# Optimization experiments

Hardware: AMD Instinct MI355X
Metric: run time of the kernel (lower is better)

## Reference

```python
import jax, jax.numpy as jnp
import numpy as np

B, N, H, DK, DV = 2, 2048, 16, 128, 128
E = H * DV
EPS = 1e-6


def setup_inputs() -> dict:
    key = jax.random.key(0)
    ks = jax.random.split(key, 8)
    sc_qk = 1.0 / np.sqrt(E + H * DK)  # xavier_normal-ish std
    sc_e = 1.0 / np.sqrt(2 * E)
    d = {
        "x": jax.random.normal(ks[0], (B, N, E), jnp.float32),
        "Wq": jax.random.normal(ks[1], (H * DK, E), jnp.float32) * sc_qk,
        "bq": jnp.zeros((H * DK,), jnp.float32),
        "Wk": jax.random.normal(ks[2], (H * DK, E), jnp.float32) * sc_qk,
        "bk": jnp.zeros((H * DK,), jnp.float32),
        "Wv": jax.random.normal(ks[3], (E, E), jnp.float32) * sc_e,
        "bv": jnp.zeros((E,), jnp.float32),
        "Wg": jax.random.normal(ks[4], (E, E), jnp.float32) * sc_e,
        "bg": jnp.zeros((E,), jnp.float32),
        "Wo": jax.random.normal(ks[5], (E, E), jnp.float32) * sc_e,
        "bo": jnp.zeros((E,), jnp.float32),
        "start_idx": 0,
    }
    return d


def _retention_scan(q, k, v, decays):
    # q,k: [B,N,H,DK] (k already scaled), v: [B,N,H,DV]
    qs = jnp.moveaxis(q, 1, 0)  # [N,B,H,DK]
    ks_ = jnp.moveaxis(k, 1, 0)
    vs = jnp.moveaxis(v, 1, 0)
    dec = decays[None, :, None, None]  # [1,H,1,1]

    def step(state, qkv):
        qt, kt, vt = qkv
        # state_n = decay * state_{n-1} + k_n (x) v_n
        state = dec * state + kt[..., :, None] * vt[..., None, :]  # [B,H,DK,DV]
        ret = jnp.einsum("bhk,bhkv->bhv", qt, state)
        return state, ret

    init = jnp.zeros((q.shape[0], H, DK, DV), q.dtype)
    final_state, rets = jax.lax.scan(step, init, (qs, ks_, vs))
    return jnp.moveaxis(rets, 0, 1), final_state  # [B,N,H,DV], [B,H,DK,DV]


def reference(x, Wq, bq, Wk, bk, Wv, bv, Wg, bg, Wo, bo, start_idx):
    b, n, _ = x.shape
    decays = 1.0 - jnp.exp2(-5.0 - jnp.arange(H, dtype=jnp.float32))  # [H]
    q = (x @ Wq.T + bq).reshape(b, n, H, DK)
    k = (x @ Wk.T + bk).reshape(b, n, H, DK) / (DK ** 0.5)
    v = (x @ Wv.T + bv).reshape(b, n, H, DV)
    retention, state = _retention_scan(q, k, v, decays)
    # GroupNorm over (b n) tokens, num_groups=H, channels=E, no affine
    r = retention.reshape(b * n, H, DV).astype(jnp.float32)
    mu = jnp.mean(r, axis=-1, keepdims=True)
    var = jnp.var(r, axis=-1, keepdims=True)
    r = (r - mu) / jnp.sqrt(var + EPS)
    r = r.reshape(b, n, E).astype(x.dtype)
    gate = jax.nn.silu(x @ Wg.T + bg)
    out = (r * gate) @ Wo.T + bo
    return out, state
```

## Files before the change

### kernel.cpp

```cpp
#include <hip/hip_runtime.h>
#include <hip/hip_bf16.h>

typedef __attribute__((ext_vector_type(8))) short short8;
typedef __attribute__((ext_vector_type(4))) short short4v;
typedef __attribute__((ext_vector_type(4))) float floatx4;

#define DI __device__ __forceinline__

constexpr int B_ = 2, N_ = 2048, H_ = 16, DK_ = 128, DV_ = 128, E_ = 2048;
constexpr int M_ = B_ * N_;
constexpr int NCAT_ = 4 * E_;
constexpr int CH_ = 128;
constexpr int NC_ = N_ / CH_;
constexpr float KSCALE = 0.08838834764831845f;

constexpr long OFF_XB   = 0;
constexpr long OFF_WCAT = 16777216;
constexpr long OFF_WOB  = 50331648;
constexpr long OFF_BCAT = 58720256;
constexpr long OFF_Y    = 58753024;
constexpr long OFF_KT   = 125861888;
constexpr long OFF_VT   = 142639104;
constexpr long OFF_SCB  = 159416320;

DI unsigned short f2bf(float f){
  unsigned u = __float_as_uint(f);
  u += 0x7fffu + ((u >> 16) & 1u);
  return (unsigned short)(u >> 16);
}
DI float bf2f(unsigned short s){ return __uint_as_float(((unsigned)s) << 16); }

DI void gload_lds16(const void* g, void* l){
  __builtin_amdgcn_global_load_lds(
      (const __attribute__((address_space(1))) unsigned int*)g,
      (__attribute__((address_space(3))) unsigned int*)l, 16, 0, 0);
}

__global__ void k_castall(const float* __restrict__ x,
                          const float* __restrict__ Wq, const float* __restrict__ Wk,
                          const float* __restrict__ Wv, const float* __restrict__ Wg,
                          const float* __restrict__ Wo,
                          const float* __restrict__ bq, const float* __restrict__ bk,
                          const float* __restrict__ bv, const float* __restrict__ bg,
                          unsigned short* __restrict__ xb, unsigned short* __restrict__ Wcat,
                          unsigned short* __restrict__ Wob, float* __restrict__ bcat){
  int bid = blockIdx.x;
  if(bid >= 14336){
    int i = (bid - 14336) * 2048 + threadIdx.x * 8;
    #pragma unroll
    for(int u=0;u<8;++u){
      int j = i + u;
      float v;
      if(j < 2048)      v = bq[j];
      else if(j < 4096) v = bk[j - 2048];
      else if(j < 6144) v = bv[j - 4096];
      else              v = bg[j - 6144];
      bcat[j] = v;
    }
    return;
  }
  const float* s; unsigned short* d; long off;
  if(bid < 4096){ s = x; d = xb; off = (long)bid*2048; }
  else if(bid < 6144){ s = Wq; d = Wcat;            off = (long)(bid-4096)*2048; }
  else if(bid < 8192){ s = Wk; d = Wcat + 4194304L; off = (long)(bid-6144)*2048; }
  else if(bid < 10240){ s = Wv; d = Wcat + 8388608L; off = (long)(bid-8192)*2048; }
  else if(bid < 12288){ s = Wg; d = Wcat + 12582912L; off = (long)(bid-10240)*2048; }
  else { s = Wo; d = Wob; off = (long)(bid-12288)*2048; }
  long i = off + (long)threadIdx.x * 8;
  float4 v0 = *(const float4*)(s + i);
  float4 v1 = *(const float4*)(s + i + 4);
  short8 o;
  o[0]=(short)f2bf(v0.x); o[1]=(short)f2bf(v0.y); o[2]=(short)f2bf(v0.z); o[3]=(short)f2bf(v0.w);
  o[4]=(short)f2bf(v1.x); o[5]=(short)f2bf(v1.y); o[6]=(short)f2bf(v1.z); o[7]=(short)f2bf(v1.w);
  *(short8*)(d + i) = o;
}

__global__ __launch_bounds__(512, 2)
void k_gemm256(const unsigned short* __restrict__ A,
               const unsigned short* __restrict__ Bt,
               unsigned short* __restrict__ Y,
               const float* __restrict__ bias)
{
  extern __shared__ unsigned short lds[];
  constexpr int K = 2048;
  constexpr int NKT = K / 64;

  const int tid = threadIdx.x;
  const int wave = tid >> 6, lane = tid & 63;
  const int wr = wave >> 2, wc = wave & 3;
  const int l15 = lane & 15;

  int bid = blockIdx.x;
  int g = bid & 7, w = bid >> 3;
  int bm = (g & 1) * 8 + (w & 7);
  int bn = (g >> 1) * 8 + (w >> 3);

  const unsigned short* Ag = A  + (long)bm * 256 * K;
  const unsigned short* Bg = Bt + (long)bn * 256 * K;

  const int sr = (lane >> 3);
  const int sc = ((lane & 7) ^ sr) * 8;
  const int colx[2] = { ((0 + (lane>>4)) ^ (lane&7)) << 4,
                        ((4 + (lane>>4)) ^ (lane&7)) << 4 };

  floatx4 acc[8][4] = {};
  const char* ldsc = (const char*)lds;

  short8 Aa[8], Ab[8], Ba[4], Bb[4];

#define STG(buf, kt) do{                                                              \
    _Pragma("unroll")                                                                 \
    for(int s=0;s<4;++s){                                                             \
      const int _i = wave*4 + s;                                                      \
      gload_lds16(Ag + (long)(_i*8 + sr)*K + (long)(kt)*64 + sc,                      \
                  &lds[(buf)*16384 + _i*512 + lane*8]);                               \
      gload_lds16(Bg + (long)(_i*8 + sr)*K + (long)(kt)*64 + sc,                      \
                  &lds[32768 + (buf)*16384 + _i*512 + lane*8]);                       \
    }                                                                                 \
  }while(0)

#define RD_A(dst, cbuf, mh) do{                                                       \
    const char* _b = ldsc + (cbuf)*32768;                                             \
    _Pragma("unroll")                                                                 \
    for(int ai=0;ai<4;++ai){                                                          \
      const int _rb = (wr*128 + (mh)*64 + ai*16 + l15) << 7;                          \
      dst[ai*2+0] = *(const short8*)(_b + _rb + colx[0]);                             \
      dst[ai*2+1] = *(const short8*)(_b + _rb + colx[1]);                             \
    }                                                                                 \
  }while(0)

#define RD_B(dst, cbuf, nh) do{                                                       \
    const char* _b = ldsc + 65536 + (cbuf)*32768;                                     \
    _Pragma("unroll")                                                                 \
    for(int bj=0;bj<2;++bj){                                                          \
      const int _rb = (wc*64 + (nh)*32 + bj*16 + l15) << 7;                           \
      dst[bj*2+0] = *(const short8*)(_b + _rb + colx[0]);                             \
      dst[bj*2+1] = *(const short8*)(_b + _rb + colx[1]);                             \
    }                                                                                 \
  }while(0)

#define MFQ(mh, nh, As, Bs) do{                                                       \
    __builtin_amdgcn_s_setprio(1);                                                    \
    _Pragma("unroll")                                                                 \
    for(int ai=0;ai<4;++ai)                                                           \
      _Pragma("unroll")                                                               \
      for(int bj=0;bj<2;++bj)                                                         \
        _Pragma("unroll")                                                             \
        for(int kk=0;kk<2;++kk)                                                       \
          acc[(mh)*4+ai][(nh)*2+bj] = __builtin_amdgcn_mfma_f32_16x16x32_bf16(        \
              As[ai*2+kk], Bs[bj*2+kk], acc[(mh)*4+ai][(nh)*2+bj], 0,0,0);            \
    __builtin_amdgcn_s_setprio(0);                                                    \
  }while(0)

#define SBAR  __builtin_amdgcn_s_barrier()
#define SCHED __builtin_amdgcn_sched_barrier(0)

  STG(0, 0);
  STG(1, 1);
  asm volatile("s_waitcnt vmcnt(8)" ::: "memory");
  SBAR;
  RD_A(Aa, 0, 0);
  RD_B(Ba, 0, 0);
  SCHED;

  #pragma unroll 1
  for(int u=0; u<NKT; ++u){
    const int cur = u & 1, nxt = cur ^ 1;

    RD_A(Ab, cur, 1);
    RD_B(Bb, cur, 1);
    SCHED;
    SBAR;
    MFQ(0, 0, Aa, Ba);
    SBAR; SCHED;

    MFQ(0, 1, Aa, Bb);
    SBAR; SCHED;

    MFQ(1, 0, Ab, Ba);
    asm volatile("s_waitcnt vmcnt(0)" ::: "memory");
    SBAR; SCHED;

    STG(cur, (u + 2) & (NKT - 1));
    RD_A(Aa, nxt, 0);
    RD_B(Ba, nxt, 0);
    SCHED;
    MFQ(1, 1, Ab, Bb);
    SCHED;
  }
#undef STG
#undef RD_A
#undef RD_B
#undef MFQ
#undef SBAR
#undef SCHED

  #pragma unroll
  for(int mh=0;mh<2;++mh){
    #pragma unroll
    for(int ai=0;ai<4;++ai){
      const int rowi = bm*256 + wr*128 + mh*64 + ai*16 + ((lane>>4)<<2);
      #pragma unroll
      for(int nh=0;nh<2;++nh){
        #pragma unroll
        for(int bj=0;bj<2;++bj){
          const int col = bn*256 + wc*64 + nh*32 + bj*16 + l15;
          const float bs = bias[col];
          const int sec = col >> 11;
          #pragma unroll
          for(int r=0;r<4;++r){
            float v = acc[mh*4+ai][nh*2+bj][r] + bs;
            if(sec == 1) v *= KSCALE;
            else if(sec == 3) v = v / (1.f + __expf(-v));
            Y[(long)(rowi + r) * NCAT_ + col] = f2bf(v);
          }
        }
      }
    }
  }
}

template<int EPI>
__global__ __launch_bounds__(256)
void k_gemm(const unsigned short* __restrict__ A,
            const unsigned short* __restrict__ Bt,
            void* __restrict__ outp,
            const float* __restrict__ bias,
            int M, int Ncols, int K, int NB)
{
  __shared__ unsigned short lA[2*128*64];
  __shared__ unsigned short lB[2*128*64];
  const int bid = blockIdx.x;
  const int bm = bid / NB, bn = bid % NB;
  const int tid = threadIdx.x;
  const int wave = tid >> 6, lane = tid & 63;
  const int wr = wave >> 1, wc = wave & 1;

  floatx4 acc[4][4] = {};

  int srow[4], scol[4];
  #pragma unroll
  for(int is=0; is<4; ++is){
    int o = is*4096 + wave*1024 + lane*16;
    int row = o >> 7;
    int logcb = (o & 127) ^ ((row & 7) << 4);
    srow[is] = row; scol[is] = logcb >> 1;
  }
  const unsigned short* Abase = A + (long)bm * 128 * K;
  const unsigned short* Bbase = Bt + (long)bn * 128 * K;

#define STG128(kt, buf) do{                                                          \
    const int _k0 = (kt) << 6;                                                       \
    _Pragma("unroll")                                                                \
    for(int is=0; is<4; ++is){                                                       \
      gload_lds16(Abase + (long)srow[is]*K + _k0 + scol[is], &lA[(buf)*8192 + ((is*4096 + wave*1024) >> 1)]); \
      gload_lds16(Bbase + (long)srow[is]*K + _k0 + scol[is], &lB[(buf)*8192 + ((is*4096 + wave*1024) >> 1)]); \
    }                                                                                \
  }while(0)

  const int nkt = K >> 6;
  STG128(0, 0);
  for(int kt=0; kt<nkt; ++kt){
    const int cur = kt & 1, nxt = cur ^ 1;
    const int ktn = (kt + 1 == nkt) ? 0 : kt + 1;
    __syncthreads();
    STG128(ktn, nxt);
    const char* cA = (const char*)lA + cur*16384;
    const char* cB = (const char*)lB + cur*16384;
    #pragma unroll
    for(int kk=0; kk<2; ++kk){
      const int cb = (kk<<6) + ((lane>>4)<<4);
      short8 af[4], bfr[4];
      #pragma unroll
      for(int i=0;i<4;++i){
        int row = (wr<<6) + (i<<4) + (lane&15);
        af[i] = *(const short8*)(cA + (row<<7) + (cb ^ ((row&7)<<4)));
      }
      #pragma unroll
      for(int j=0;j<4;++j){
        int row = (wc<<6) + (j<<4) + (lane&15);
        bfr[j] = *(const short8*)(cB + (row<<7) + (cb ^ ((row&7)<<4)));
      }
      #pragma unroll
      for(int i=0;i<4;++i)
        #pragma unroll
        for(int j=0;j<4;++j)
          acc[i][j] = __builtin_amdgcn_mfma_f32_16x16x32_bf16(af[i], bfr[j], acc[i][j], 0,0,0);
    }
  }
#undef STG128

  #pragma unroll
  for(int i=0;i<4;++i){
    #pragma unroll
    for(int j=0;j<4;++j){
      #pragma unroll
      for(int r=0;r<4;++r){
        int row = bm*128 + (wr<<6) + (i<<4) + ((lane>>4)<<2) + r;
        int col = bn*128 + (wc<<6) + (j<<4) + (lane&15);
        float v = acc[i][j][r] + bias[col];
        if(EPI == 0){
          int sec = col >> 11;
          if(sec == 1) v *= KSCALE;
          else if(sec == 3) v = v / (1.f + __expf(-v));
          ((unsigned short*)outp)[(long)row * Ncols + col] = f2bf(v);
        } else {
          ((float*)outp)[(long)row * Ncols + col] = v;
        }
      }
    }
  }
}

__global__ __launch_bounds__(256)
void k_transpose(const unsigned short* __restrict__ Y,
                 unsigned short* __restrict__ Kt, unsigned short* __restrict__ Vt){
  __shared__ unsigned short lt[128][136];
  int bid = blockIdx.x;
  int op = bid >> 9;
  int r  = bid & 511;
  int bh = r >> 4, c = r & 15, b = bh >> 4, h = bh & 15;
  int tid = threadIdx.x;
  float dec = 1.f - exp2f(-5.f - (float)h);
  float l2d = log2f(dec);
  int sec = op ? 4096 : 2048;
  unsigned short* Dst = op ? Vt : Kt;

  #pragma unroll
  for(int p=0;p<8;++p){
    int t = p*16 + (tid>>4);
    long src = ((long)(b*N_ + c*CH_ + t)) * NCAT_ + sec + h*128 + (tid&15)*8;
    short8 v = *(const short8*)(Y + src);
    if(op == 0){
      float f = exp2f(-(float)t * l2d);
      #pragma unroll
      for(int u=0;u<8;++u) v[u] = (short)f2bf(bf2f((unsigned short)v[u]) * f);
    }
    *(short8*)&lt[t][(tid&15)*8] = v;
  }
  __syncthreads();
  #pragma unroll
  for(int p=0;p<8;++p){
    int dk = p*16 + (tid>>4);
    int tc = (tid&15)*8;
    short8 o;
    #pragma unroll
    for(int u=0;u<8;++u) o[u] = (short)lt[tc+u][dk];
    *(short8*)(Dst + ((long)(bh*128 + dk)) * N_ + c*CH_ + tc) = o;
  }
}

__global__ __launch_bounds__(256)
void k_chunksum(const unsigned short* __restrict__ Ktd, const unsigned short* __restrict__ Vt,
                float* __restrict__ MS){
  int bid = blockIdx.x;
  int bh = bid >> 4, c = bid & 15, h = bh & 15;
  int tid = threadIdx.x, wave = tid >> 6, lane = tid & 63;
  int wr = wave >> 1, wc = wave & 1;
  floatx4 acc[4][4] = {};
  const unsigned short* Vb = Vt  + (long)bh*128*N_ + c*CH_;
  const unsigned short* Kb = Ktd + (long)bh*128*N_ + c*CH_;

  #pragma unroll
  for(int kk=0;kk<4;++kk){
    int tl = kk*32 + ((lane>>4)<<3);
    short8 af[4], bfr[4];
    #pragma unroll
    for(int i=0;i<4;++i){ int dv = (wr<<6)+(i<<4)+(lane&15); af[i]  = *(const short8*)(Vb + (long)dv*N_ + tl); }
    #pragma unroll
    for(int j=0;j<4;++j){ int dk = (wc<<6)+(j<<4)+(lane&15); bfr[j] = *(const short8*)(Kb + (long)dk*N_ + tl); }
    #pragma unroll
    for(int i=0;i<4;++i)
      #pragma unroll
      for(int j=0;j<4;++j)
        acc[i][j] = __builtin_amdgcn_mfma_f32_16x16x32_bf16(af[i], bfr[j], acc[i][j], 0,0,0);
  }
  float dec = 1.f - exp2f(-5.f - (float)h);
  float scale = exp2f(127.f * log2f(dec));
  float* Mo = MS + ((long)bh*NC_ + c) * 16384;
  #pragma unroll
  for(int i=0;i<4;++i)
    #pragma unroll
    for(int j=0;j<4;++j)
      #pragma unroll
      for(int r=0;r<4;++r){
        int dv = (wr<<6)+(i<<4)+((lane>>4)<<2)+r;
        int dk = (wc<<6)+(j<<4)+(lane&15);
        Mo[dv*128 + dk] = acc[i][j][r] * scale;
      }
}

__global__ __launch_bounds__(256)
void k_scan(const float* __restrict__ MS, unsigned short* __restrict__ Scb,
            float* __restrict__ stateOut){
  int bid = blockIdx.x;
  int bh = bid >> 4, p = bid & 15;
  int tid = threadIdx.x, h = bh & 15;
  float dec = 1.f - exp2f(-5.f - (float)h);
  float decC = exp2f(128.f * log2f(dec));
  int e0 = p*1024 + tid*4;
  floatx4 S = {0.f, 0.f, 0.f, 0.f};
  const float* base = MS + (long)bh * NC_ * 16384 + e0;
  unsigned short* sb = Scb + (long)bh * NC_ * 16384 + e0;
  for(int c=0;c<NC_;++c){
    floatx4 m = *(const floatx4*)(base + (long)c*16384);
    short4v q;
    #pragma unroll
    for(int u=0;u<4;++u) q[u] = (short)f2bf(S[u]);
    *(short4v*)(sb + (long)c*16384) = q;
    S = decC * S + m;
  }
  int dv = e0 >> 7, dk = e0 & 127;
  float* so = stateOut + (long)bh*16384 + dv;
  #pragma unroll
  for(int u=0;u<4;++u) so[(long)(dk+u)*128] = S[u];
}

__global__ __launch_bounds__(256)
void k_ret(const unsigned short* __restrict__ Y, const unsigned short* __restrict__ Vt,
           const unsigned short* __restrict__ Scb, unsigned short* __restrict__ RG){
  __shared__ unsigned short sQ[128*128];
  __shared__ unsigned short sK[128*128];
  int bid = blockIdx.x;
  int bh = bid >> 4, c = bid & 15, b = bh >> 4, h = bh & 15;
  int tid = threadIdx.x, w = tid >> 6, lane = tid & 63;
  float dec = 1.f - exp2f(-5.f - (float)h);
  float l2d = log2f(dec);

  #pragma unroll
  for(int p=0;p<8;++p){
    int t = p*16 + (tid>>4);
    long row = (long)(b*N_ + c*CH_ + t) * NCAT_ + h*128 + (tid&15)*8;
    short8 qv = *(const short8*)(Y + row);
    short8 kv = *(const short8*)(Y + row + 2048);
    float fq = exp2f((float)t * l2d);
    float fk = exp2f(-(float)t * l2d);
    short8 qs, ks;
    #pragma unroll
    for(int u=0;u<8;++u){
      qs[u] = (short)f2bf(bf2f((unsigned short)qv[u]) * fq);
      ks[u] = (short)f2bf(bf2f((unsigned short)kv[u]) * fk);
    }
    int ad = t*256 + (((tid&15)*16) ^ ((t&7)<<4));
    *(short8*)((char*)sQ + ad) = qs;
    *(short8*)((char*)sK + ad) = ks;
  }
  __syncthreads();

  floatx4 acc[2][8] = {};
  #pragma unroll
  for(int kk=0;kk<4;++kk){
    int cb = (kk<<6) + ((lane>>4)<<4);
    short8 af[2], bfr[8];
    #pragma unroll
    for(int i=0;i<2;++i){ int t = w*32 + (i<<4) + (lane&15); af[i] = *(const short8*)((const char*)sQ + t*256 + (cb ^ ((t&7)<<4))); }
    #pragma unroll
    for(int j=0;j<8;++j){ int s = (j<<4) + (lane&15); bfr[j] = *(const short8*)((const char*)sK + s*256 + (cb ^ ((s&7)<<4))); }
    #pragma unroll
    for(int i=0;i<2;++i)
      #pragma unroll
      for(int j=0;j<8;++j)
        acc[i][j] = __builtin_amdgcn_mfma_f32_16x16x32_bf16(af[i], bfr[j], acc[i][j], 0,0,0);
  }
  __syncthreads();

  #pragma unroll
  for(int i=0;i<2;++i)
    #pragma unroll
    for(int j=0;j<8;++j)
      #pragma unroll
      for(int r=0;r<4;++r){
        int t = w*32 + (i<<4) + ((lane>>4)<<2) + r;
        int s = (j<<4) + (lane&15);
        float v = (s <= t) ? acc[i][j][r] : 0.f;
        *(unsigned short*)((char*)sK + t*256 + ((s*2) ^ ((t&7)<<4))) = f2bf(v);
      }
  __syncthreads();

  #pragma unroll
  for(int i=0;i<2;++i)
    #pragma unroll
    for(int j=0;j<8;++j)
      #pragma unroll
      for(int u=0;u<4;++u) acc[i][j][u] = 0.f;

  const unsigned short* Vb = Vt + (long)bh*128*N_ + c*CH_;
  #pragma unroll
  for(int kk=0;kk<4;++kk){
    int cb = (kk<<6) + ((lane>>4)<<4);
    int sg = kk*32 + ((lane>>4)<<3);
    short8 af[2], bfr[8];
    #pragma unroll
    for(int i=0;i<2;++i){ int t = w*32 + (i<<4) + (lane&15); af[i] = *(const short8*)((const char*)sK + t*256 + (cb ^ ((t&7)<<4))); }
    #pragma unroll
    for(int j=0;j<8;++j){ int dv = (j<<4) + (lane&15); bfr[j] = *(const short8*)(Vb + (long)dv*N_ + sg); }
    #pragma unroll
    for(int i=0;i<2;++i)
      #pragma unroll
      for(int j=0;j<8;++j)
        acc[i][j] = __builtin_amdgcn_mfma_f32_16x16x32_bf16(af[i], bfr[j], acc[i][j], 0,0,0);
  }
  const unsigned short* Sb = Scb + ((long)bh*NC_ + c) * 16384;
  #pragma unroll
  for(int kk=0;kk<4;++kk){
    int cb = (kk<<6) + ((lane>>4)<<4);
    int kg = kk*32 + ((lane>>4)<<3);
    short8 af[2], bfr[8];
    #pragma unroll
    for(int i=0;i<2;++i){
      int t = w*32 + (i<<4) + (lane&15);
      short8 qv = *(const short8*)((const char*)sQ + t*256 + (cb ^ ((t&7)<<4)));
      #pragma unroll
      for(int u=0;u<8;++u) af[i][u] = (short)f2bf(bf2f((unsigned short)qv[u]) * dec);
    }
    #pragma unroll
    for(int j=0;j<8;++j){ int dv = (j<<4) + (lane&15); bfr[j] = *(const short8*)(Sb + (long)dv*128 + kg); }
    #pragma unroll
    for(int i=0;i<2;++i)
      #pragma unroll
      for(int j=0;j<8;++j)
        acc[i][j] = __builtin_amdgcn_mfma_f32_16x16x32_bf16(af[i], bfr[j], acc[i][j], 0,0,0);
  }

  #pragma unroll
  for(int i=0;i<2;++i){
    #pragma unroll
    for(int r=0;r<4;++r){
      float s1 = 0.f, s2 = 0.f;
      #pragma unroll
      for(int j=0;j<8;++j){ float v = acc[i][j][r]; s1 += v; s2 += v*v; }
      #pragma unroll
      for(int off=1; off<16; off<<=1){ s1 += __shfl_xor(s1, off); s2 += __shfl_xor(s2, off); }
      float mu  = s1 * (1.f/128.f);
      float var = s2 * (1.f/128.f) - mu*mu;
      float inv = rsqrtf(var + 1e-6f);
      int t = w*32 + (i<<4) + ((lane>>4)<<2) + r;
      long mrow = (long)(b*N_ + c*CH_ + t);
      #pragma unroll
      for(int j=0;j<8;++j){
        int dv = (j<<4) + (lane&15);
        float v = (acc[i][j][r] - mu) * inv;
        float g = bf2f(Y[mrow*NCAT_ + 6144 + h*128 + dv]);
        RG[mrow*E_ + h*128 + dv] = f2bf(v * g);
      }
    }
  }
}

extern "C" void kernel_launch(void* const* d_in, const int* in_sizes, int n_in,
                              void* d_out, int out_size, void* d_ws, size_t ws_size,
                              hipStream_t stream) {
  const float* x  = (const float*)d_in[0];
  const float* Wq = (const float*)d_in[1];
  const float* bq = (const float*)d_in[2];
  const float* Wk = (const float*)d_in[3];
  const float* bk = (const float*)d_in[4];
  const float* Wv = (const float*)d_in[5];
  const float* bv = (const float*)d_in[6];
  const float* Wg = (const float*)d_in[7];
  const float* bg = (const float*)d_in[8];
  const float* Wo = (const float*)d_in[9];
  const float* bo = (const float*)d_in[10];

  char* ws = (char*)d_ws;
  unsigned short* xb   = (unsigned short*)(ws + OFF_XB);
  unsigned short* Wcat = (unsigned short*)(ws + OFF_WCAT);
  unsigned short* Wob  = (unsigned short*)(ws + OFF_WOB);
  float*          bcat = (float*)(ws + OFF_BCAT);
  unsigned short* Y    = (unsigned short*)(ws + OFF_Y);
  unsigned short* Ktd  = (unsigned short*)(ws + OFF_KT);
  unsigned short* Vt   = (unsigned short*)(ws + OFF_VT);
  unsigned short* Scb  = (unsigned short*)(ws + OFF_SCB);
  float*          MS   = (float*)(ws + OFF_WCAT);
  unsigned short* RG   = (unsigned short*)(ws + OFF_XB);

  float* outp     = (float*)d_out;
  float* stateOut = outp + (long)M_ * E_;

  (void)hipFuncSetAttribute((const void*)k_gemm256,
                            hipFuncAttributeMaxDynamicSharedMemorySize, 131072);

  k_castall<<<14340, 256, 0, stream>>>(x, Wq, Wk, Wv, Wg, Wo, bq, bk, bv, bg,
                                       xb, Wcat, Wob, bcat);

  k_gemm256<<<512, 512, 131072, stream>>>(xb, Wcat, Y, bcat);

  k_transpose<<<1024, 256, 0, stream>>>(Y, Ktd, Vt);

  k_chunksum<<<512, 256, 0, stream>>>(Ktd, Vt, MS);
  k_scan<<<512, 256, 0, stream>>>(MS, Scb, stateOut);
  k_ret<<<512, 256, 0, stream>>>(Y, Vt, Scb, RG);

  k_gemm<1><<<(M_/128)*(E_/128), 256, 0, stream>>>(RG, Wob, (void*)outp, bo, M_, E_, E_, E_/128);
}
```

Measured before the change: 282.9 us.

## Split GEMM tile loads into quarter stages interleaved with MFMA quadrants

After: 281.1 us. Within noise of the previous version (-0.6%).

```diff
diff --git a/kernel.cpp b/kernel.cpp
--- a/kernel.cpp
+++ b/kernel.cpp
@@ -105,35 +105,42 @@
 
   floatx4 acc[8][4] = {};
   const char* ldsc = (const char*)lds;
-
   short8 Aa[8], Ab[8], Ba[4], Bb[4];
 
-#define STG(buf, kt) do{                                                              \
+#define STG_A(buf, kt, mh) do{                                                        \
     _Pragma("unroll")                                                                 \
-    for(int s=0;s<4;++s){                                                             \
-      const int _i = wave*4 + s;                                                      \
-      gload_lds16(Ag + (long)(_i*8 + sr)*K + (long)(kt)*64 + sc,                      \
-                  &lds[(buf)*16384 + _i*512 + lane*8]);                               \
-      gload_lds16(Bg + (long)(_i*8 + sr)*K + (long)(kt)*64 + sc,                      \
-                  &lds[32768 + (buf)*16384 + _i*512 + lane*8]);                       \
+    for(int g2=0; g2<2; ++g2){                                                        \
+      gload_lds16(Ag + (long)(wr*128 + (mh)*64 + wc*16 + g2*8 + sr)*K                 \
+                     + (long)(kt)*64 + sc,                                            \
+                  &lds[(buf)*16384 + wr*8192 + ((mh)*64 + wc*16 + g2*8)*64 + lane*8]);\
     }                                                                                 \
   }while(0)
 
-#define RD_A(dst, cbuf, mh) do{                                                       \
-    const char* _b = ldsc + (cbuf)*32768;                                             \
+#define STG_B(buf, kt, nh) do{                                                        \
     _Pragma("unroll")                                                                 \
-    for(int ai=0;ai<4;++ai){                                                          \
-      const int _rb = (wr*128 + (mh)*64 + ai*16 + l15) << 7;                          \
+    for(int g2=0; g2<2; ++g2){                                                        \
+      gload_lds16(Bg + (long)(wc*64 + (nh)*32 + wr*16 + g2*8 + sr)*K                  \
+                     + (long)(kt)*64 + sc,                                            \
+                  &lds[32768 + (buf)*16384 + (wc>>1)*8192                             \
+                       + ((wc&1)*64 + (nh)*32 + wr*16 + g2*8)*64 + lane*8]);          \
+    }                                                                                 \
+  }while(0)
+
+#define RD_A(dst, buf, mh) do{                                                        \
+    const char* _b = ldsc + ((buf)*16384 + wr*8192)*2;                                \
+    _Pragma("unroll")                                                                 \
+    for(int ai=0; ai<4; ++ai){                                                        \
+      const int _rb = ((mh)*64 + ai*16 + l15) << 7;                                   \
       dst[ai*2+0] = *(const short8*)(_b + _rb + colx[0]);                             \
       dst[ai*2+1] = *(const short8*)(_b + _rb + colx[1]);                             \
     }                                                                                 \
   }while(0)
 
-#define RD_B(dst, cbuf, nh) do{                                                       \
-    const char* _b = ldsc + 65536 + (cbuf)*32768;                                     \
+#define RD_B(dst, buf, nh) do{                                                        \
+    const char* _b = ldsc + (32768 + (buf)*16384 + (wc>>1)*8192)*2;                   \
     _Pragma("unroll")                                                                 \
-    for(int bj=0;bj<2;++bj){                                                          \
-      const int _rb = (wc*64 + (nh)*32 + bj*16 + l15) << 7;                           \
+    for(int bj=0; bj<2; ++bj){                                                        \
+      const int _rb = ((wc&1)*64 + (nh)*32 + bj*16 + l15) << 7;                       \
       dst[bj*2+0] = *(const short8*)(_b + _rb + colx[0]);                             \
       dst[bj*2+1] = *(const short8*)(_b + _rb + colx[1]);                             \
     }                                                                                 \
@@ -142,57 +149,75 @@
 #define MFQ(mh, nh, As, Bs) do{                                                       \
     __builtin_amdgcn_s_setprio(1);                                                    \
     _Pragma("unroll")                                                                 \
-    for(int ai=0;ai<4;++ai)                                                           \
+    for(int ai=0; ai<4; ++ai)                                                         \
       _Pragma("unroll")                                                               \
-      for(int bj=0;bj<2;++bj)                                                         \
+      for(int bj=0; bj<2; ++bj)                                                       \
         _Pragma("unroll")                                                             \
-        for(int kk=0;kk<2;++kk)                                                       \
+        for(int kk=0; kk<2; ++kk)                                                     \
           acc[(mh)*4+ai][(nh)*2+bj] = __builtin_amdgcn_mfma_f32_16x16x32_bf16(        \
               As[ai*2+kk], Bs[bj*2+kk], acc[(mh)*4+ai][(nh)*2+bj], 0,0,0);            \
     __builtin_amdgcn_s_setprio(0);                                                    \
   }while(0)
 
-#define SBAR  __builtin_amdgcn_s_barrier()
+#define VM4   asm volatile("s_waitcnt vmcnt(4)" ::: "memory")
+#define BAR   __builtin_amdgcn_s_barrier()
 #define SCHED __builtin_amdgcn_sched_barrier(0)
 
-  STG(0, 0);
-  STG(1, 1);
-  asm volatile("s_waitcnt vmcnt(8)" ::: "memory");
-  SBAR;
-  RD_A(Aa, 0, 0);
-  RD_B(Ba, 0, 0);
+  STG_A(0, 0, 0); STG_B(0, 0, 0); STG_B(0, 0, 1); STG_A(0, 0, 1);
+  VM4;
+  BAR;
   SCHED;
 
   #pragma unroll 1
-  for(int u=0; u<NKT; ++u){
-    const int cur = u & 1, nxt = cur ^ 1;
-
-    RD_A(Ab, cur, 1);
-    RD_B(Bb, cur, 1);
-    SCHED;
-    SBAR;
+  for(int i=0; i<NKT/2; ++i){
+    const int t1 = 2*i + 1;
+    const int t2 = (2*i + 2) & (NKT - 1);
+
+    RD_A(Aa, 0, 0); RD_B(Ba, 0, 0);
+    STG_A(1, t1, 0); STG_B(1, t1, 0);
+    VM4; BAR;
     MFQ(0, 0, Aa, Ba);
-    SBAR; SCHED;
-
+    BAR; SCHED;
+    RD_B(Bb, 0, 1);
+    STG_B(1, t1, 1);
+    VM4; BAR;
     MFQ(0, 1, Aa, Bb);
-    SBAR; SCHED;
-
+    BAR; SCHED;
+    RD_A(Ab, 0, 1);
+    STG_A(1, t1, 1);
+    VM4; BAR;
+    MFQ(1, 1, Ab, Bb);
+    BAR; SCHED;
+    VM4; BAR;
     MFQ(1, 0, Ab, Ba);
-    asm volatile("s_waitcnt vmcnt(0)" ::: "memory");
-    SBAR; SCHED;
-
-    STG(cur, (u + 2) & (NKT - 1));
-    RD_A(Aa, nxt, 0);
-    RD_B(Ba, nxt, 0);
-    SCHED;
+    BAR; SCHED;
+
+    RD_A(Aa, 1, 0); RD_B(Ba, 1, 0);
+    STG_A(0, t2, 0); STG_B(0, t2, 0);
+    VM4; BAR;
+    MFQ(0, 0, Aa, Ba);
+    BAR; SCHED;
+    RD_B(Bb, 1, 1);
+    STG_B(0, t2, 1);
+    VM4; BAR;
+    MFQ(0, 1, Aa, Bb);
+    BAR; SCHED;
+    RD_A(Ab, 1, 1);
+    STG_A(0, t2, 1);
+    VM4; BAR;
     MFQ(1, 1, Ab, Bb);
-    SCHED;
-  }
-#undef STG
+    BAR; SCHED;
+    VM4; BAR;
+    MFQ(1, 0, Ab, Ba);
+    BAR; SCHED;
+  }
+#undef STG_A
+#undef STG_B
 #undef RD_A
 #undef RD_B
 #undef MFQ
-#undef SBAR
+#undef VM4
+#undef BAR
 #undef SCHED
 
   #pragma unroll
```
